# Kernel tuning notes

Hardware: AMD Instinct MI355X
Metric: run time of the kernel (lower is better)

The kernel has to match this reference:

```python
import jax, jax.numpy as jnp
import numpy as np

N_SEQ, MAX_LEN, H_DIM, N_CHAR = 8, 4096, 1024, 256


def setup_inputs() -> dict:
    key = jax.random.key(0)
    ks = jax.random.split(key, 10)
    n_char_ev = 32768
    L, E = 12, 16384
    char_i_seq = jax.random.randint(ks[0], (n_char_ev,), 0, N_SEQ)
    char_i_pos = jax.random.randint(ks[1], (n_char_ev,), 0, MAX_LEN)
    char_ids = jax.random.randint(ks[2], (n_char_ev,), 0, N_CHAR)
    grp_i_seq = jax.random.randint(ks[3], (L, E), 0, N_SEQ)
    grp_i_first = jax.random.randint(ks[4], (L, E), 0, MAX_LEN)
    grp_i_second = jax.random.randint(ks[5], (L, E), 0, MAX_LEN)
    grp_i_pos = jax.random.randint(ks[6], (L, E), 0, MAX_LEN)
    # Learned params: embedding table (std = 1/sqrt(h_dim)) and composer Linear(2h -> h)
    emb_char = jax.random.normal(ks[7], (N_CHAR, H_DIM), dtype=jnp.float32) * (1.0 / H_DIM ** 0.5)
    W = jax.random.normal(ks[8], (2 * H_DIM, H_DIM), dtype=jnp.float32) * (1.0 / (2 * H_DIM) ** 0.5)
    b = jnp.zeros((H_DIM,), dtype=jnp.float32)
    return {"char_i_seq": char_i_seq, "char_i_pos": char_i_pos, "char_ids": char_ids,
            "grp_i_seq": grp_i_seq, "grp_i_first": grp_i_first, "grp_i_second": grp_i_second,
            "grp_i_pos": grp_i_pos, "emb_char": emb_char, "W": W, "b": b}


def reference(char_i_seq, char_i_pos, char_ids, grp_i_seq, grp_i_first,
              grp_i_second, grp_i_pos, emb_char, W, b):
    # h_frag: [n_seq, max_len, h_dim]
    h = jnp.zeros((N_SEQ, MAX_LEN, H_DIM), dtype=emb_char.dtype)
    # Leaf characters: embedding lookup + scatter-add
    h = h.at[char_i_seq, char_i_pos].add(emb_char[char_ids])

    def composer(left, right):
        # tanh(Linear(concat(left, right))) : [E, 2h] @ [2h, h] -> [E, h]
        return jnp.tanh(jnp.concatenate([left, right], axis=-1) @ W + b)

    def level_step(h, idx):
        i_seq, i_first, i_second, i_pos = idx
        out = composer(h[i_seq, i_first], h[i_seq, i_second])  # gather -> compose
        return h.at[i_seq, i_pos].add(out), None                # scatter-add

    h, _ = jax.lax.scan(level_step, h, (grp_i_seq, grp_i_first, grp_i_second, grp_i_pos))
    h = h.at[:, 0].set(0.0)  # h_frag[:, 0].fill_(0)
    return h
```

## Files before the change

### kernel.cpp

```cpp
#include <hip/hip_runtime.h>

#define NS 8
#define ML 4096
#define HD 1024
#define K2 2048
#define NEV 32768
#define NLEV 12
#define NE 16384
#define NSLOT (NS * ML)
#define CAP 8
#define BK 64

typedef __attribute__((ext_vector_type(8))) short bf16x8;
typedef __attribute__((ext_vector_type(4))) float f32x4;

typedef __attribute__((address_space(1))) const void cvoid_g;
typedef __attribute__((address_space(3))) void void_l;

static __device__ __forceinline__ void load_lds_16(const void* g, void* l) {
    __builtin_amdgcn_global_load_lds((cvoid_g*)g, (void_l*)l, 16, 0, 0);
}

static __device__ __forceinline__ unsigned short f2bf(float f) {
    unsigned u = __float_as_uint(f);
    unsigned r = (u + 0x7fffu + ((u >> 16) & 1u)) >> 16;
    return (unsigned short)r;
}

static __device__ __forceinline__ float fast_tanh(float x) {
    return 1.0f - 2.0f / (__expf(2.0f * x) + 1.0f);
}

__global__ void wt_kernel(const float* __restrict__ W, unsigned short* __restrict__ WbT) {
    __shared__ unsigned short tile[64][65];
    const int t = threadIdx.x;
    const int k0 = blockIdx.x * 64;
    const int n0 = blockIdx.y * 64;
#pragma unroll
    for (int i = 0; i < 16; i++) {
        int idx = i * 256 + t;
        int r = idx >> 6, c = idx & 63;
        tile[r][c] = f2bf(W[(size_t)(k0 + r) * HD + n0 + c]);
    }
    __syncthreads();
#pragma unroll
    for (int i = 0; i < 16; i++) {
        int idx = i * 256 + t;
        int r = idx >> 6, c = idx & 63;
        WbT[(size_t)(n0 + r) * K2 + k0 + c] = tile[c][r];
    }
}

__global__ void char_ticket(const int* __restrict__ cseq, const int* __restrict__ cpos,
                            int* __restrict__ counts, int* __restrict__ ticket,
                            int* __restrict__ evlist) {
    const int e = blockIdx.x * 256 + threadIdx.x;
    if (e >= NEV) return;
    const int slot = cseq[e] * ML + cpos[e];
    const int t = atomicAdd(&counts[slot], 1);
    ticket[e] = t;
    if (t < CAP) evlist[slot * CAP + t] = e;
}

__global__ void char_slot_sum(const int* __restrict__ counts, const int* __restrict__ evlist,
                              const int* __restrict__ cid, const float* __restrict__ emb,
                              float* __restrict__ h) {
    const int slot = blockIdx.x;
    const int t = threadIdx.x;
    int n = counts[slot];
    if (n > CAP) n = CAP;
    float4 acc = {0.f, 0.f, 0.f, 0.f};
    for (int i = 0; i < n; i++) {
        const int e = evlist[slot * CAP + i];
        const int id = cid[e];
        const float4 v = ((const float4*)(emb + (size_t)id * HD))[t];
        acc.x += v.x; acc.y += v.y; acc.z += v.z; acc.w += v.w;
    }
    ((float4*)(h + (size_t)slot * HD))[t] = acc;
}

__global__ void char_overflow(const int* __restrict__ cseq, const int* __restrict__ cpos,
                              const int* __restrict__ cid, const int* __restrict__ ticket,
                              const float* __restrict__ emb, float* __restrict__ h) {
    const int e0 = blockIdx.x * 128;
    const int t = threadIdx.x;
    for (int i = 0; i < 128; i++) {
        const int e = e0 + i;
        if (ticket[e] < CAP) continue;
        const int slot = cseq[e] * ML + cpos[e];
        const int id = cid[e];
        const float4 v = ((const float4*)(emb + (size_t)id * HD))[t];
        float* dst = h + (size_t)slot * HD + t * 4;
        atomicAdd(dst + 0, v.x);
        atomicAdd(dst + 1, v.y);
        atomicAdd(dst + 2, v.z);
        atomicAdd(dst + 3, v.w);
    }
}

__global__ void grp_count(const int* __restrict__ iseq, const int* __restrict__ ipos,
                          int* __restrict__ gcounts) {
    const int idx = blockIdx.x * 256 + threadIdx.x;
    if (idx >= NLEV * NE) return;
    const int lev = idx >> 14;
    atomicAdd(&gcounts[lev * NSLOT + iseq[idx] * ML + ipos[idx]], 1);
}

__global__ void grp_dup(const int* __restrict__ iseq, const int* __restrict__ ipos,
                        const int* __restrict__ gcounts, unsigned char* __restrict__ dup) {
    const int idx = blockIdx.x * 256 + threadIdx.x;
    if (idx >= NLEV * NE) return;
    const int lev = idx >> 14;
    dup[idx] = (gcounts[lev * NSLOT + iseq[idx] * ML + ipos[idx]] > 1) ? 1 : 0;
}

__global__ void gather_x(const float* __restrict__ h, const int* __restrict__ iseq,
                         const int* __restrict__ ifirst, const int* __restrict__ isecond,
                         unsigned short* __restrict__ X) {
    const int e = blockIdx.x;
    const int t = threadIdx.x;
    const int seq = iseq[e], f = ifirst[e], s = isecond[e];
    const float4 a = ((const float4*)(h + ((size_t)seq * ML + f) * HD))[t];
    const float4 b = ((const float4*)(h + ((size_t)seq * ML + s) * HD))[t];
    ushort4 pa, pb;
    pa.x = f2bf(a.x); pa.y = f2bf(a.y); pa.z = f2bf(a.z); pa.w = f2bf(a.w);
    pb.x = f2bf(b.x); pb.y = f2bf(b.y); pb.z = f2bf(b.z); pb.w = f2bf(b.w);
    *(ushort4*)(X + (size_t)e * K2 + t * 4) = pa;
    *(ushort4*)(X + (size_t)e * K2 + HD + t * 4) = pb;
}

__global__ __launch_bounds__(256, 3) void gemm_scatter(
    const unsigned short* __restrict__ X,
    const unsigned short* __restrict__ WbT,
    const float* __restrict__ bias,
    const int* __restrict__ iseq, const int* __restrict__ ipos,
    const unsigned char* __restrict__ dup,
    float* __restrict__ h) {
    __shared__ unsigned short sA[128 * BK];
    __shared__ unsigned short sB[128 * BK];
    const int t = threadIdx.x;
    const int lane = t & 63;
    const int w = t >> 6;
    const int wm = (w >> 1) * 64, wn = (w & 1) * 64;
    const int fr = lane & 15, fq = lane >> 4;
    const int row0 = blockIdx.x * 128;
    const int col0 = blockIdx.y * 128;

    f32x4 acc[4][4];
#pragma unroll
    for (int i = 0; i < 4; i++)
#pragma unroll
        for (int j = 0; j < 4; j++) acc[i][j] = (f32x4){0.f, 0.f, 0.f, 0.f};

    const int sr = t >> 3;
    const int sp = (t & 7) ^ (sr & 7);
    const unsigned short* Asrc = X + (size_t)(row0 + sr) * K2 + sp * 8;
    const unsigned short* Bsrc = WbT + (size_t)(col0 + sr) * K2 + sp * 8;

    const int s7 = fr & 7;

    for (int k0 = 0; k0 < K2; k0 += BK) {
#pragma unroll
        for (int i = 0; i < 4; i++) {
            const int c = i * 256 + t;
            load_lds_16(Asrc + (size_t)i * 32 * K2 + k0, &sA[c * 8]);
            load_lds_16(Bsrc + (size_t)i * 32 * K2 + k0, &sB[c * 8]);
        }
        __syncthreads();
#pragma unroll
        for (int pass = 0; pass < 2; pass++) {
            const int q = pass * 4 + fq;
            const int qs = (q ^ s7) * 8;
            bf16x8 af[4], bfr[4];
#pragma unroll
            for (int mt = 0; mt < 4; mt++)
                af[mt] = *(const bf16x8*)&sA[(wm + mt * 16 + fr) * BK + qs];
#pragma unroll
            for (int nt = 0; nt < 4; nt++)
                bfr[nt] = *(const bf16x8*)&sB[(wn + nt * 16 + fr) * BK + qs];
#pragma unroll
            for (int mt = 0; mt < 4; mt++)
#pragma unroll
                for (int nt = 0; nt < 4; nt++)
                    acc[mt][nt] = __builtin_amdgcn_mfma_f32_16x16x32_bf16(
                        af[mt], bfr[nt], acc[mt][nt], 0, 0, 0);
        }
        __syncthreads();
    }

    float bv[4];
#pragma unroll
    for (int nt = 0; nt < 4; nt++) bv[nt] = bias[col0 + wn + nt * 16 + fr];
#pragma unroll
    for (int mt = 0; mt < 4; mt++) {
#pragma unroll
        for (int r = 0; r < 4; r++) {
            const int e = row0 + wm + mt * 16 + fq * 4 + r;
            const int seq = iseq[e], pos = ipos[e];
            float* hrow = h + ((size_t)seq * ML + pos) * HD + col0 + wn;
            const bool d = dup[e] != 0;
            if (d) {
#pragma unroll
                for (int nt = 0; nt < 4; nt++) {
                    float x = fast_tanh(acc[mt][nt][r] + bv[nt]);
                    atomicAdd(&hrow[nt * 16 + fr], x);
                }
            } else {
#pragma unroll
                for (int nt = 0; nt < 4; nt++) {
                    float x = fast_tanh(acc[mt][nt][r] + bv[nt]);
                    hrow[nt * 16 + fr] += x;
                }
            }
        }
    }
}

__global__ void zero_first(float* __restrict__ h) {
    const int t = blockIdx.x * 256 + threadIdx.x;
    const int seq = t >> 10, d = t & 1023;
    h[(size_t)seq * ML * HD + d] = 0.0f;
}

extern "C" void kernel_launch(void* const* d_in, const int* in_sizes, int n_in,
                              void* d_out, int out_size, void* d_ws, size_t ws_size,
                              hipStream_t stream) {
    const int* char_i_seq = (const int*)d_in[0];
    const int* char_i_pos = (const int*)d_in[1];
    const int* char_ids   = (const int*)d_in[2];
    const int* grp_i_seq    = (const int*)d_in[3];
    const int* grp_i_first  = (const int*)d_in[4];
    const int* grp_i_second = (const int*)d_in[5];
    const int* grp_i_pos    = (const int*)d_in[6];
    const float* emb = (const float*)d_in[7];
    const float* W   = (const float*)d_in[8];
    const float* b   = (const float*)d_in[9];
    float* h = (float*)d_out;

    unsigned short* WbT = (unsigned short*)d_ws;
    unsigned short* X   = (unsigned short*)((char*)d_ws + (8u << 20));
    int* counts = (int*)((char*)d_ws + (72u << 20));
    int* ticket = (int*)((char*)d_ws + (72u << 20) + (1u << 18));
    int* evlist = (int*)((char*)d_ws + (72u << 20) + (1u << 19));
    int* gcounts = (int*)((char*)d_ws + (74u << 20));
    unsigned char* gdup = (unsigned char*)((char*)d_ws + (76u << 20));

    hipMemsetAsync(counts, 0, NSLOT * sizeof(int), stream);
    hipMemsetAsync(gcounts, 0, (size_t)NLEV * NSLOT * sizeof(int), stream);
    wt_kernel<<<dim3(32, 16), 256, 0, stream>>>(W, WbT);
    char_ticket<<<NEV / 256, 256, 0, stream>>>(char_i_seq, char_i_pos, counts, ticket, evlist);
    char_slot_sum<<<NSLOT, 256, 0, stream>>>(counts, evlist, char_ids, emb, h);
    char_overflow<<<NEV / 128, 256, 0, stream>>>(char_i_seq, char_i_pos, char_ids, ticket, emb, h);
    grp_count<<<(NLEV * NE) / 256, 256, 0, stream>>>(grp_i_seq, grp_i_pos, gcounts);
    grp_dup<<<(NLEV * NE) / 256, 256, 0, stream>>>(grp_i_seq, grp_i_pos, gcounts, gdup);

    for (int lev = 0; lev < NLEV; lev++) {
        const int* iseq = grp_i_seq + lev * NE;
        const int* ifir = grp_i_first + lev * NE;
        const int* isec = grp_i_second + lev * NE;
        const int* ipos = grp_i_pos + lev * NE;
        gather_x<<<NE, 256, 0, stream>>>(h, iseq, ifir, isec, X);
        gemm_scatter<<<dim3(128, 8), 256, 0, stream>>>(X, WbT, b, iseq, ipos,
                                                       gdup + lev * NE, h);
    }
    zero_first<<<32, 256, 0, stream>>>(h);
}
```

Measured before the change: 1.741 ms.

## Use 256x256 double-buffered GEMM tiles with XCD-aware block mapping

Replaces the 128x128 single-buffered GEMM with a 256x256 tile per 512-thread block, using 128 KB of dynamic LDS split into two buffers so the next K-slice loads while the current one feeds MFMAs. Blocks are mapped so that blocks on the same XCD share row and column panels, and s_setprio raises wave priority around the MFMA bursts. Larger tiles cut global and L2 traffic per FLOP. The cost is fewer blocks (256), heavier register pressure from 32 accumulators per thread, and reliance on hand-written vmcnt waits.

```diff
diff --git a/kernel.cpp b/kernel.cpp
--- a/kernel.cpp
+++ b/kernel.cpp
@@ -10,6 +10,8 @@
 #define NSLOT (NS * ML)
 #define CAP 8
 #define BK 64
+#define NT (K2 / BK)
+#define LDS_BYTES 131072
 
 typedef __attribute__((ext_vector_type(8))) short bf16x8;
 typedef __attribute__((ext_vector_type(4))) float f32x4;
@@ -129,87 +131,122 @@
     *(ushort4*)(X + (size_t)e * K2 + HD + t * 4) = pb;
 }
 
-__global__ __launch_bounds__(256, 3) void gemm_scatter(
+__global__ __launch_bounds__(512, 2) void gemm_scatter(
     const unsigned short* __restrict__ X,
     const unsigned short* __restrict__ WbT,
     const float* __restrict__ bias,
     const int* __restrict__ iseq, const int* __restrict__ ipos,
     const unsigned char* __restrict__ dup,
     float* __restrict__ h) {
-    __shared__ unsigned short sA[128 * BK];
-    __shared__ unsigned short sB[128 * BK];
+    extern __shared__ unsigned short lds[];
     const int t = threadIdx.x;
     const int lane = t & 63;
     const int w = t >> 6;
-    const int wm = (w >> 1) * 64, wn = (w & 1) * 64;
+    const int wm = w >> 2;
+    const int wn = (w & 3) * 64;
     const int fr = lane & 15, fq = lane >> 4;
-    const int row0 = blockIdx.x * 128;
-    const int col0 = blockIdx.y * 128;
-
-    f32x4 acc[4][4];
-#pragma unroll
-    for (int i = 0; i < 4; i++)
+
+    const int bid = blockIdx.x;
+    const int xcd = bid & 7, bix = bid >> 3;
+    const int row0 = ((xcd & 1) * 32 + bix) * 256;
+    const int col0 = (xcd >> 1) * 256;
+
+    const int tr = t >> 3;
+    const int sp = (t & 7) ^ (tr & 7);
+    const unsigned short* Asrc = X + (size_t)(row0 + tr) * K2 + sp * 8;
+    const unsigned short* Bsrc = WbT + (size_t)(col0 + tr) * K2 + sp * 8;
+
+    f32x4 acc[8][4];
+#pragma unroll
+    for (int i = 0; i < 8; i++)
 #pragma unroll
         for (int j = 0; j < 4; j++) acc[i][j] = (f32x4){0.f, 0.f, 0.f, 0.f};
 
-    const int sr = t >> 3;
-    const int sp = (t & 7) ^ (sr & 7);
-    const unsigned short* Asrc = X + (size_t)(row0 + sr) * K2 + sp * 8;
-    const unsigned short* Bsrc = WbT + (size_t)(col0 + sr) * K2 + sp * 8;
-
-    const int s7 = fr & 7;
-
-    for (int k0 = 0; k0 < K2; k0 += BK) {
-#pragma unroll
-        for (int i = 0; i < 4; i++) {
-            const int c = i * 256 + t;
-            load_lds_16(Asrc + (size_t)i * 32 * K2 + k0, &sA[c * 8]);
-            load_lds_16(Bsrc + (size_t)i * 32 * K2 + k0, &sB[c * 8]);
+    {
+        unsigned short* dA = lds;
+        unsigned short* dB = lds + 16384;
+#pragma unroll
+        for (int i = 0; i < 4; i++)
+            load_lds_16(Asrc + (size_t)(i * 64) * K2, &dA[(i * 512 + t) * 8]);
+#pragma unroll
+        for (int i = 0; i < 4; i++)
+            load_lds_16(Bsrc + (size_t)(i * 64) * K2, &dB[(i * 512 + t) * 8]);
+    }
+
+    for (int kt = 0; kt < NT; kt++) {
+        const int d = kt & 1;
+        if (kt + 1 < NT) {
+            unsigned short* dA = lds + (d ^ 1) * 32768;
+            unsigned short* dB = dA + 16384;
+            const size_t ko = (size_t)(kt + 1) * BK;
+#pragma unroll
+            for (int i = 0; i < 4; i++)
+                load_lds_16(Asrc + (size_t)(i * 64) * K2 + ko, &dA[(i * 512 + t) * 8]);
+#pragma unroll
+            for (int i = 0; i < 4; i++)
+                load_lds_16(Bsrc + (size_t)(i * 64) * K2 + ko, &dB[(i * 512 + t) * 8]);
+            asm volatile("s_waitcnt vmcnt(8)" ::: "memory");
+        } else {
+            asm volatile("s_waitcnt vmcnt(0)" ::: "memory");
         }
-        __syncthreads();
-#pragma unroll
-        for (int pass = 0; pass < 2; pass++) {
-            const int q = pass * 4 + fq;
-            const int qs = (q ^ s7) * 8;
-            bf16x8 af[4], bfr[4];
-#pragma unroll
-            for (int mt = 0; mt < 4; mt++)
-                af[mt] = *(const bf16x8*)&sA[(wm + mt * 16 + fr) * BK + qs];
-#pragma unroll
-            for (int nt = 0; nt < 4; nt++)
-                bfr[nt] = *(const bf16x8*)&sB[(wn + nt * 16 + fr) * BK + qs];
-#pragma unroll
-            for (int mt = 0; mt < 4; mt++)
-#pragma unroll
-                for (int nt = 0; nt < 4; nt++)
-                    acc[mt][nt] = __builtin_amdgcn_mfma_f32_16x16x32_bf16(
-                        af[mt], bfr[nt], acc[mt][nt], 0, 0, 0);
+        __builtin_amdgcn_s_barrier();
+        asm volatile("" ::: "memory");
+
+        const unsigned short* sA = lds + d * 32768;
+        const unsigned short* sB = sA + 16384;
+#pragma unroll
+        for (int q = 0; q < 4; q++) {
+            const int mh = (q & 1) * 64;
+            const int nh = (q >> 1) * 32;
+            bf16x8 af[2][4], bfr[2][2];
+#pragma unroll
+            for (int ks = 0; ks < 2; ks++) {
+                const int qs = ((ks * 4 + fq) ^ (fr & 7)) * 8;
+#pragma unroll
+                for (int mt = 0; mt < 4; mt++)
+                    af[ks][mt] = *(const bf16x8*)&sA[(wm * 128 + mh + mt * 16 + fr) * BK + qs];
+#pragma unroll
+                for (int nt = 0; nt < 2; nt++)
+                    bfr[ks][nt] = *(const bf16x8*)&sB[(wn + nh + nt * 16 + fr) * BK + qs];
+            }
+            __builtin_amdgcn_s_setprio(1);
+#pragma unroll
+            for (int ks = 0; ks < 2; ks++)
+#pragma unroll
+                for (int mt = 0; mt < 4; mt++)
+#pragma unroll
+                    for (int nt = 0; nt < 2; nt++)
+                        acc[(q & 1) * 4 + mt][(q >> 1) * 2 + nt] =
+                            __builtin_amdgcn_mfma_f32_16x16x32_bf16(
+                                af[ks][mt], bfr[ks][nt],
+                                acc[(q & 1) * 4 + mt][(q >> 1) * 2 + nt], 0, 0, 0);
+            __builtin_amdgcn_s_setprio(0);
         }
-        __syncthreads();
+        asm volatile("" ::: "memory");
+        __builtin_amdgcn_s_barrier();
     }
 
     float bv[4];
 #pragma unroll
-    for (int nt = 0; nt < 4; nt++) bv[nt] = bias[col0 + wn + nt * 16 + fr];
-#pragma unroll
-    for (int mt = 0; mt < 4; mt++) {
+    for (int ni = 0; ni < 4; ni++) bv[ni] = bias[col0 + wn + ni * 16 + fr];
+#pragma unroll
+    for (int mi = 0; mi < 8; mi++) {
 #pragma unroll
         for (int r = 0; r < 4; r++) {
-            const int e = row0 + wm + mt * 16 + fq * 4 + r;
+            const int e = row0 + wm * 128 + mi * 16 + fq * 4 + r;
             const int seq = iseq[e], pos = ipos[e];
             float* hrow = h + ((size_t)seq * ML + pos) * HD + col0 + wn;
-            const bool d = dup[e] != 0;
-            if (d) {
-#pragma unroll
-                for (int nt = 0; nt < 4; nt++) {
-                    float x = fast_tanh(acc[mt][nt][r] + bv[nt]);
-                    atomicAdd(&hrow[nt * 16 + fr], x);
+            if (dup[e]) {
+#pragma unroll
+                for (int ni = 0; ni < 4; ni++) {
+                    float x = fast_tanh(acc[mi][ni][r] + bv[ni]);
+                    atomicAdd(&hrow[ni * 16 + fr], x);
                 }
             } else {
 #pragma unroll
-                for (int nt = 0; nt < 4; nt++) {
-                    float x = fast_tanh(acc[mt][nt][r] + bv[nt]);
-                    hrow[nt * 16 + fr] += x;
+                for (int ni = 0; ni < 4; ni++) {
+                    float x = fast_tanh(acc[mi][ni][r] + bv[ni]);
+                    hrow[ni * 16 + fr] += x;
                 }
             }
         }
@@ -245,6 +282,13 @@
     int* gcounts = (int*)((char*)d_ws + (74u << 20));
     unsigned char* gdup = (unsigned char*)((char*)d_ws + (76u << 20));
 
+    static bool attr_done = false;
+    if (!attr_done) {
+        (void)hipFuncSetAttribute((const void*)gemm_scatter,
+                                  hipFuncAttributeMaxDynamicSharedMemorySize, LDS_BYTES);
+        attr_done = true;
+    }
+
     hipMemsetAsync(counts, 0, NSLOT * sizeof(int), stream);
     hipMemsetAsync(gcounts, 0, (size_t)NLEV * NSLOT * sizeof(int), stream);
     wt_kernel<<<dim3(32, 16), 256, 0, stream>>>(W, WbT);
@@ -260,8 +304,8 @@
         const int* isec = grp_i_second + lev * NE;
         const int* ipos = grp_i_pos + lev * NE;
         gather_x<<<NE, 256, 0, stream>>>(h, iseq, ifir, isec, X);
-        gemm_scatter<<<dim3(128, 8), 256, 0, stream>>>(X, WbT, b, iseq, ipos,
-                                                       gdup + lev * NE, h);
+        gemm_scatter<<<dim3(256), 512, LDS_BYTES, stream>>>(X, WbT, b, iseq, ipos,
+                                                            gdup + lev * NE, h);
     }
     zero_first<<<32, 256, 0, stream>>>(h);
 }
```

Measured after the change: 1.630 ms. 6.4% less time.
